# Kernel optimization log

Measured on AMD Instinct MI355X. Metric: run time of the kernel, lower is better.

## Reference

```python
import jax, jax.numpy as jnp
import numpy as np

N, E = 20000, 200000
HID, NH, L = 128, 8, 7
DH = HID // NH
SCALE = float(np.sqrt(DH))
NNUM = 5
MLP_IN = HID + HID + 8 + 8 + 8 + NNUM  # 285
EPS = 1e-5


def _ln(x, g, b):
    mu = jnp.mean(x, -1, keepdims=True)
    var = jnp.mean((x - mu) ** 2, -1, keepdims=True)
    return (x - mu) * jax.lax.rsqrt(var + EPS) * g + b


def setup_inputs() -> dict:
    key = jax.random.key(0)
    ks = jax.random.split(key, 24)
    f = lambda k, s: (0.05 * jax.random.normal(k, s)).astype(jnp.float32)
    z = lambda s: jnp.zeros(s, jnp.float32)
    o = lambda s: jnp.ones(s, jnp.float32)
    inp = {
        'node_feats': f(ks[0], (N, 2)),
        'numericals': f(ks[1], (E, NNUM)),
        'W_emb': f(ks[2], (2, HID)), 'b_emb': z((HID,)),
        'WQ': f(ks[3], (L, HID, HID)), 'bQ': z((L, HID)),
        'WK': f(ks[4], (L, HID, HID)), 'bK': z((L, HID)),
        'WV': f(ks[5], (L, HID, HID)), 'bV': z((L, HID)),
        'WO': f(ks[6], (L, HID, HID)), 'bO': z((L, HID)),
        'ln1_g': o((L, HID)), 'ln1_b': z((L, HID)),
        'ln2_g': o((L, HID)), 'ln2_b': z((L, HID)),
        'W1': f(ks[7], (L, HID, HID)), 'b1': z((L, HID)),
        'W2': f(ks[8], (L, HID, HID)), 'b2': z((L, HID)),
        'curr_emb': f(ks[9], (15, 8)), 'pay_emb': f(ks[10], (7, 8)),
        'mlp_Wh': f(ks[11], (3, MLP_IN, MLP_IN)), 'mlp_bh': z((3, MLP_IN)),
        'mlp_Wo': f(ks[12], (MLP_IN, 2)), 'mlp_bo': z((2,)),
        'src': jax.random.randint(ks[13], (E,), 0, N, dtype=jnp.int32),
        'dst': jax.random.randint(ks[14], (E,), 0, N, dtype=jnp.int32),
        'payment_currency': jax.random.randint(ks[15], (E,), 0, 15, dtype=jnp.int32),
        'receiving_currency': jax.random.randint(ks[16], (E,), 0, 15, dtype=jnp.int32),
        'payment_format': jax.random.randint(ks[17], (E,), 0, 7, dtype=jnp.int32),
    }
    return inp


def reference(node_feats, numericals, W_emb, b_emb, WQ, bQ, WK, bK, WV, bV, WO, bO,
              ln1_g, ln1_b, ln2_g, ln2_b, W1, b1, W2, b2, curr_emb, pay_emb,
              mlp_Wh, mlp_bh, mlp_Wo, mlp_bo, src, dst,
              payment_currency, receiving_currency, payment_format):
    h = node_feats @ W_emb + b_emb  # [N, HID]
    for l in range(L):
        # --- graph multi-head attention (segment softmax over in-edges of dst) ---
        x = _ln(h, ln1_g[l], ln1_b[l])
        Q = (x @ WQ[l] + bQ[l]).reshape(N, NH, DH)
        K = (x @ WK[l] + bK[l]).reshape(N, NH, DH)
        V = (x @ WV[l] + bV[l]).reshape(N, NH, DH)
        scores = jnp.einsum('ehd,ehd->eh', Q[dst], K[src]) / SCALE  # [E, NH]
        m = jax.ops.segment_max(scores, dst, num_segments=N)        # [N, NH]
        ex = jnp.exp(scores - m[dst])
        den = jax.ops.segment_sum(ex, dst, num_segments=N)
        w = ex / den[dst]                                           # attn weights per edge
        attn = jax.ops.segment_sum(w[:, :, None] * V[src], dst, num_segments=N)
        h = h + attn.reshape(N, HID) @ WO[l] + bO[l]
        # --- FFN ---
        x = _ln(h, ln2_g[l], ln2_b[l])
        h = h + jax.nn.relu(x @ W1[l] + b1[l]) @ W2[l] + b2[l]
    # --- edge classifier ---
    ef = jnp.concatenate([curr_emb[payment_currency], curr_emb[receiving_currency],
                          pay_emb[payment_format], numericals], axis=1)  # [E, 29]
    y = jnp.concatenate([h[src], h[dst], ef], axis=1)  # [E, 285]
    for i in range(3):
        y = jax.nn.relu(y @ mlp_Wh[i] + mlp_bh[i])
    return y @ mlp_Wo + mlp_bo  # [E, 2]
```

## Files before the change

kernel.cpp:

```cpp
#include <hip/hip_runtime.h>

#define HID 128
#define NH 8
#define DH 16
#define NLAYERS 7
#define MLP_IN 285
#define MP 288
#define LDW 296
#define XS 136

typedef short short8 __attribute__((ext_vector_type(8)));
typedef float f32x4 __attribute__((ext_vector_type(4)));
typedef float f32x16 __attribute__((ext_vector_type(16)));
typedef unsigned short ushort8 __attribute__((ext_vector_type(8)));

__device__ inline unsigned short f2bf(float f) {
    union { float f; unsigned int u; } v; v.f = f;
    unsigned int r = v.u + 0x7FFF + ((v.u >> 16) & 1);
    return (unsigned short)(r >> 16);
}
__device__ inline float bf2f(unsigned short u) {
    union { unsigned int u; float f; } v; v.u = ((unsigned int)u) << 16;
    return v.f;
}

__global__ __launch_bounds__(256) void embed_kernel(
    const float* __restrict__ nf, const float* __restrict__ We,
    const float* __restrict__ be, float* __restrict__ h, int N)
{
    int idx = blockIdx.x * 256 + threadIdx.x;
    if (idx >= N * HID) return;
    int n = idx >> 7, j = idx & 127;
    h[idx] = fmaf(nf[n * 2], We[j], fmaf(nf[n * 2 + 1], We[HID + j], be[j]));
}

__global__ __launch_bounds__(256) void prep_nodew_kernel(
    const float* __restrict__ WQ, const float* __restrict__ WK,
    const float* __restrict__ WV, const float* __restrict__ WO,
    const float* __restrict__ W1, const float* __restrict__ W2,
    unsigned short* __restrict__ wnh, unsigned short* __restrict__ wnl)
{
    int idx = blockIdx.x * 256 + threadIdx.x;
    if (idx >= 42 * 32 * 64) return;
    int lane = idx & 63;
    int r = idx >> 6;
    int kt = r & 7; r >>= 3;
    int ct = r & 3; r >>= 2;
    int m = r;
    int l = m / 6, wi = m - l * 6;
    const float* Wb;
    switch (wi) {
        case 0: Wb = WQ; break; case 1: Wb = WK; break; case 2: Wb = WV; break;
        case 3: Wb = WO; break; case 4: Wb = W1; break; default: Wb = W2; break;
    }
    Wb += (size_t)l * HID * HID;
    int n = ct * 32 + (lane & 31);
    int kb = kt * 16 + (lane >> 5) * 8;
    ushort8 vh, vl;
#pragma unroll
    for (int j = 0; j < 8; ++j) {
        float w = Wb[(size_t)(kb + j) * HID + n];
        unsigned short hi = f2bf(w);
        vh[j] = hi;
        vl[j] = f2bf(w - bf2f(hi));
    }
    *(ushort8*)&wnh[(size_t)idx * 8] = vh;
    *(ushort8*)&wnl[(size_t)idx * 8] = vl;
}

#define LOADB(m, BH, BL) do { \
    size_t fb_ = (((size_t)(matbase + (m)) * 32 + (size_t)wave * 8) * 64 + lane) * 8; \
    const unsigned short* Bh_ = wnh + fb_; \
    const unsigned short* Bl_ = wnl + fb_; \
    _Pragma("unroll") \
    for (int kt = 0; kt < 8; ++kt) { \
        BH[kt] = *(const short8*)&Bh_[kt * 512]; \
        BL[kt] = *(const short8*)&Bl_[kt * 512]; \
    } \
    __builtin_amdgcn_sched_barrier(0); \
} while (0)

#define COMPSTORE(BH, BL, BIAS, OUT, STRIDE, OFF) do { \
    f32x16 acc = {}; \
    _Pragma("unroll") \
    for (int kt = 0; kt < 8; ++kt) \
        acc = __builtin_amdgcn_mfma_f32_32x32x16_bf16(ah[kt], BH[kt], acc, 0, 0, 0); \
    _Pragma("unroll") \
    for (int kt = 0; kt < 8; ++kt) \
        acc = __builtin_amdgcn_mfma_f32_32x32x16_bf16(al[kt], BH[kt], acc, 0, 0, 0); \
    _Pragma("unroll") \
    for (int kt = 0; kt < 8; ++kt) \
        acc = __builtin_amdgcn_mfma_f32_32x32x16_bf16(ah[kt], BL[kt], acc, 0, 0, 0); \
    int col_ = wave * 32 + l31; \
    float bv_ = (BIAS)[col_]; \
    _Pragma("unroll") \
    for (int r = 0; r < 16; ++r) { \
        int rowm_ = (r & 3) + 8 * (r >> 2) + 4 * half; \
        int row_ = rowBase + rowm_; \
        if (row_ < M) (OUT)[(size_t)row_ * (STRIDE) + (OFF) + col_] = acc[r] + bv_; \
    } \
} while (0)

__global__ __launch_bounds__(256, 2) void ln_qkv_mfma(
    const float* __restrict__ h,
    const float* __restrict__ g, const float* __restrict__ bb,
    const unsigned short* __restrict__ wnh, const unsigned short* __restrict__ wnl,
    int matbase,
    const float* __restrict__ bQ, const float* __restrict__ bK, const float* __restrict__ bV,
    float* __restrict__ qo, float* __restrict__ kvo, int M)
{
    __shared__ unsigned short Xh[32][XS];
    __shared__ unsigned short Xl[32][XS];
    int tid = threadIdx.x;
    int lane = tid & 63, wave = tid >> 6;
    int rowBase = blockIdx.x * 32;

    for (int i = 0; i < 8; ++i) {
        int r = wave * 8 + i;
        int row = rowBase + r;
        float a0 = 0.f, a1 = 0.f;
        if (row < M) {
            a0 = h[(size_t)row * HID + lane];
            a1 = h[(size_t)row * HID + 64 + lane];
        }
        float s = a0 + a1;
#pragma unroll
        for (int off = 32; off > 0; off >>= 1) s += __shfl_down(s, off, 64);
        s = __shfl(s, 0, 64);
        float mu = s * (1.0f / 128.0f);
        float d0 = a0 - mu, d1 = a1 - mu;
        float v = d0 * d0 + d1 * d1;
#pragma unroll
        for (int off = 32; off > 0; off >>= 1) v += __shfl_down(v, off, 64);
        v = __shfl(v, 0, 64);
        float rr = rsqrtf(v * (1.0f / 128.0f) + 1e-5f);
        float x0 = d0 * rr * g[lane] + bb[lane];
        float x1 = d1 * rr * g[64 + lane] + bb[64 + lane];
        unsigned short h0 = f2bf(x0), h1 = f2bf(x1);
        Xh[r][lane] = h0;           Xh[r][64 + lane] = h1;
        Xl[r][lane] = f2bf(x0 - bf2f(h0));
        Xl[r][64 + lane] = f2bf(x1 - bf2f(h1));
    }
    __syncthreads();

    int l31 = lane & 31;
    int half = lane >> 5;

    short8 ah[8], al[8];
#pragma unroll
    for (int kt = 0; kt < 8; ++kt) {
        ah[kt] = *(const short8*)&Xh[l31][kt * 16 + half * 8];
        al[kt] = *(const short8*)&Xl[l31][kt * 16 + half * 8];
    }

    short8 bh0[8], bl0[8], bh1[8], bl1[8];
    LOADB(0, bh0, bl0);
    LOADB(1, bh1, bl1);
    COMPSTORE(bh0, bl0, bQ, qo, HID, 0);
    LOADB(2, bh0, bl0);
    COMPSTORE(bh1, bl1, bK, kvo, 256, 0);
    COMPSTORE(bh0, bl0, bV, kvo, 256, 128);
}

__global__ __launch_bounds__(256, 2) void post_qkv_mfma(
    const float* __restrict__ at, const float* __restrict__ hin,
    const unsigned short* __restrict__ wnh, const unsigned short* __restrict__ wnl,
    int matbase,
    const float* __restrict__ bO,
    const float* __restrict__ g2, const float* __restrict__ b2g,
    const float* __restrict__ b1, const float* __restrict__ b2,
    float* __restrict__ hout,
    int doQkv,
    const float* __restrict__ g1n, const float* __restrict__ b1n,
    const float* __restrict__ bQn, const float* __restrict__ bKn, const float* __restrict__ bVn,
    float* __restrict__ qout, float* __restrict__ kvout,
    unsigned short* __restrict__ hbout,
    int M)
{
    __shared__ unsigned short Ah[32][XS];
    __shared__ unsigned short Al[32][XS];
    __shared__ unsigned short Th[32][XS];
    __shared__ unsigned short Tl[32][XS];
    __shared__ float Hs[32][132];
    int tid = threadIdx.x;
    int lane = tid & 63, wave = tid >> 6;
    int rowBase = blockIdx.x * 32;
    int l31 = lane & 31;
    int half = lane >> 5;

    for (int i = tid; i < 32 * 32; i += 256) {
        int r = i >> 5, c4 = i & 31;
        int row = rowBase + r;
        float4 va = make_float4(0.f, 0.f, 0.f, 0.f), vh = va;
        if (row < M) {
            va = *(const float4*)&at[(size_t)row * HID + c4 * 4];
            vh = *(const float4*)&hin[(size_t)row * HID + c4 * 4];
        }
        const float* vp = (const float*)&va;
#pragma unroll
        for (int q = 0; q < 4; ++q) {
            unsigned short hi = f2bf(vp[q]);
            Ah[r][c4 * 4 + q] = hi;
            Al[r][c4 * 4 + q] = f2bf(vp[q] - bf2f(hi));
        }
        *(float4*)&Hs[r][c4 * 4] = vh;
    }
    __syncthreads();

    int colW = wave * 32 + l31;

    {
        short8 ah[8], al[8];
#pragma unroll
        for (int kt = 0; kt < 8; ++kt) {
            ah[kt] = *(const short8*)&Ah[l31][kt * 16 + half * 8];
            al[kt] = *(const short8*)&Al[l31][kt * 16 + half * 8];
        }
        short8 bh[8], bl[8];
        {
            size_t fb = (((size_t)(matbase + 3) * 32 + (size_t)wave * 8) * 64 + lane) * 8;
            const unsigned short* Bh = wnh + fb;
            const unsigned short* Bl = wnl + fb;
#pragma unroll
            for (int kt = 0; kt < 8; ++kt) {
                bh[kt] = *(const short8*)&Bh[kt * 512];
                bl[kt] = *(const short8*)&Bl[kt * 512];
            }
            __builtin_amdgcn_sched_barrier(0);
        }
        f32x16 acc = {};
#pragma unroll
        for (int kt = 0; kt < 8; ++kt)
            acc = __builtin_amdgcn_mfma_f32_32x32x16_bf16(ah[kt], bh[kt], acc, 0, 0, 0);
#pragma unroll
        for (int kt = 0; kt < 8; ++kt)
            acc = __builtin_amdgcn_mfma_f32_32x32x16_bf16(al[kt], bh[kt], acc, 0, 0, 0);
#pragma unroll
        for (int kt = 0; kt < 8; ++kt)
            acc = __builtin_amdgcn_mfma_f32_32x32x16_bf16(ah[kt], bl[kt], acc, 0, 0, 0);
        float bv = bO[colW];
#pragma unroll
        for (int r = 0; r < 16; ++r) {
            int rowm = (r & 3) + 8 * (r >> 2) + 4 * half;
            Hs[rowm][colW] += acc[r] + bv;
        }
    }
    __syncthreads();

    for (int i = 0; i < 8; ++i) {
        int r = wave * 8 + i;
        float a0 = Hs[r][lane];
        float a1 = Hs[r][64 + lane];
        float s = a0 + a1;
#pragma unroll
        for (int off = 32; off > 0; off >>= 1) s += __shfl_down(s, off, 64);
        s = __shfl(s, 0, 64);
        float mu = s * (1.0f / 128.0f);
        float d0 = a0 - mu, d1 = a1 - mu;
        float v = d0 * d0 + d1 * d1;
#pragma unroll
        for (int off = 32; off > 0; off >>= 1) v += __shfl_down(v, off, 64);
        v = __shfl(v, 0, 64);
        float rr = rsqrtf(v * (1.0f / 128.0f) + 1e-5f);
        float x0 = d0 * rr * g2[lane] + b2g[lane];
        float x1 = d1 * rr * g2[64 + lane] + b2g[64 + lane];
        unsigned short h0 = f2bf(x0), h1 = f2bf(x1);
        Ah[r][lane] = h0;           Ah[r][64 + lane] = h1;
        Al[r][lane] = f2bf(x0 - bf2f(h0));
        Al[r][64 + lane] = f2bf(x1 - bf2f(h1));
    }
    __syncthreads();

    {
        short8 ah[8], al[8];
#pragma unroll
        for (int kt = 0; kt < 8; ++kt) {
            ah[kt] = *(const short8*)&Ah[l31][kt * 16 + half * 8];
            al[kt] = *(const short8*)&Al[l31][kt * 16 + half * 8];
        }
        short8 bh[8], bl[8];
        {
            size_t fb = (((size_t)(matbase + 4) * 32 + (size_t)wave * 8) * 64 + lane) * 8;
            const unsigned short* Bh = wnh + fb;
            const unsigned short* Bl = wnl + fb;
#pragma unroll
            for (int kt = 0; kt < 8; ++kt) {
                bh[kt] = *(const short8*)&Bh[kt * 512];
                bl[kt] = *(const short8*)&Bl[kt * 512];
            }
            __builtin_amdgcn_sched_barrier(0);
        }
        f32x16 acc = {};
#pragma unroll
        for (int kt = 0; kt < 8; ++kt)
            acc = __builtin_amdgcn_mfma_f32_32x32x16_bf16(ah[kt], bh[kt], acc, 0, 0, 0);
#pragma unroll
        for (int kt = 0; kt < 8; ++kt)
            acc = __builtin_amdgcn_mfma_f32_32x32x16_bf16(al[kt], bh[kt], acc, 0, 0, 0);
#pragma unroll
        for (int kt = 0; kt < 8; ++kt)
            acc = __builtin_amdgcn_mfma_f32_32x32x16_bf16(ah[kt], bl[kt], acc, 0, 0, 0);
        float bv = b1[colW];
#pragma unroll
        for (int r = 0; r < 16; ++r) {
            int rowm = (r & 3) + 8 * (r >> 2) + 4 * half;
            float t = fmaxf(acc[r] + bv, 0.f);
            unsigned short hi = f2bf(t);
            Th[rowm][colW] = hi;
            Tl[rowm][colW] = f2bf(t - bf2f(hi));
        }
    }
    __syncthreads();

    {
        short8 ah[8], al[8];
#pragma unroll
        for (int kt = 0; kt < 8; ++kt) {
            ah[kt] = *(const short8*)&Th[l31][kt * 16 + half * 8];
            al[kt] = *(const short8*)&Tl[l31][kt * 16 + half * 8];
        }
        short8 bh[8], bl[8];
        {
            size_t fb = (((size_t)(matbase + 5) * 32 + (size_t)wave * 8) * 64 + lane) * 8;
            const unsigned short* Bh = wnh + fb;
            const unsigned short* Bl = wnl + fb;
#pragma unroll
            for (int kt = 0; kt < 8; ++kt) {
                bh[kt] = *(const short8*)&Bh[kt * 512];
                bl[kt] = *(const short8*)&Bl[kt * 512];
            }
            __builtin_amdgcn_sched_barrier(0);
        }
        f32x16 acc = {};
#pragma unroll
        for (int kt = 0; kt < 8; ++kt)
            acc = __builtin_amdgcn_mfma_f32_32x32x16_bf16(ah[kt], bh[kt], acc, 0, 0, 0);
#pragma unroll
        for (int kt = 0; kt < 8; ++kt)
            acc = __builtin_amdgcn_mfma_f32_32x32x16_bf16(al[kt], bh[kt], acc, 0, 0, 0);
#pragma unroll
        for (int kt = 0; kt < 8; ++kt)
            acc = __builtin_amdgcn_mfma_f32_32x32x16_bf16(ah[kt], bl[kt], acc, 0, 0, 0);
        float bv = b2[colW];
#pragma unroll
        for (int r = 0; r < 16; ++r) {
            int rowm = (r & 3) + 8 * (r >> 2) + 4 * half;
            int row = rowBase + rowm;
            float hn = Hs[rowm][colW] + acc[r] + bv;
            Hs[rowm][colW] = hn;
            if (row < M) {
                if (doQkv) hout[(size_t)row * HID + colW] = hn;
                else       hbout[(size_t)row * HID + colW] = f2bf(hn);
            }
        }
    }

    if (!doQkv) return;
    __syncthreads();

    for (int i = 0; i < 8; ++i) {
        int r = wave * 8 + i;
        float a0 = Hs[r][lane];
        float a1 = Hs[r][64 + lane];
        float s = a0 + a1;
#pragma unroll
        for (int off = 32; off > 0; off >>= 1) s += __shfl_down(s, off, 64);
        s = __shfl(s, 0, 64);
        float mu = s * (1.0f / 128.0f);
        float d0 = a0 - mu, d1 = a1 - mu;
        float v = d0 * d0 + d1 * d1;
#pragma unroll
        for (int off = 32; off > 0; off >>= 1) v += __shfl_down(v, off, 64);
        v = __shfl(v, 0, 64);
        float rr = rsqrtf(v * (1.0f / 128.0f) + 1e-5f);
        float x0 = d0 * rr * g1n[lane] + b1n[lane];
        float x1 = d1 * rr * g1n[64 + lane] + b1n[64 + lane];
        unsigned short h0 = f2bf(x0), h1 = f2bf(x1);
        Ah[r][lane] = h0;           Ah[r][64 + lane] = h1;
        Al[r][lane] = f2bf(x0 - bf2f(h0));
        Al[r][64 + lane] = f2bf(x1 - bf2f(h1));
    }
    __syncthreads();

    {
        short8 ah[8], al[8];
#pragma unroll
        for (int kt = 0; kt < 8; ++kt) {
            ah[kt] = *(const short8*)&Ah[l31][kt * 16 + half * 8];
            al[kt] = *(const short8*)&Al[l31][kt * 16 + half * 8];
        }
        short8 bh0[8], bl0[8], bh1[8], bl1[8];
        LOADB(6, bh0, bl0);
        LOADB(7, bh1, bl1);
        COMPSTORE(bh0, bl0, bQn, qout, HID, 0);
        LOADB(8, bh0, bl0);
        COMPSTORE(bh1, bl1, bKn, kvout, 256, 0);
        COMPSTORE(bh0, bl0, bVn, kvout, 256, 128);
    }
}

__global__ __launch_bounds__(256) void deg_kernel(
    const int* __restrict__ dst, int* __restrict__ deg, int E)
{
    int e = blockIdx.x * 256 + threadIdx.x;
    if (e < E) atomicAdd(&deg[dst[e]], 1);
}

__global__ __launch_bounds__(256) void scan_kernel(
    const int* __restrict__ deg, int* __restrict__ rowptr,
    int* __restrict__ cursor, int N)
{
    __shared__ int sums[256];
    int tid = threadIdx.x;
    int chunk = (N + 255) / 256;
    int lo = tid * chunk;
    int hi = lo + chunk; if (hi > N) hi = N;
    int s = 0;
    for (int i = lo; i < hi && i >= 0; ++i) s += deg[i];
    sums[tid] = s;
    __syncthreads();
    for (int off = 1; off < 256; off <<= 1) {
        int v = (tid >= off) ? sums[tid - off] : 0;
        __syncthreads();
        sums[tid] += v;
        __syncthreads();
    }
    int base = (tid == 0) ? 0 : sums[tid - 1];
    for (int i = lo; i < hi; ++i) {
        rowptr[i] = base; cursor[i] = base; base += deg[i];
    }
    if (tid == 255) rowptr[N] = sums[255];
}

__global__ __launch_bounds__(256) void scatter_kernel(
    const int* __restrict__ src, const int* __restrict__ dst,
    int* __restrict__ cursor, int* __restrict__ ssrc, int E)
{
    int e = blockIdx.x * 256 + threadIdx.x;
    if (e < E) {
        int p = atomicAdd(&cursor[dst[e]], 1);
        ssrc[p] = src[e];
    }
}

__global__ __launch_bounds__(256) void attn_fused_kernel(
    const float* __restrict__ q, const float* __restrict__ kv,
    const int* __restrict__ rowptr, const int* __restrict__ ssrc,
    float* __restrict__ at, int N)
{
    int node = blockIdx.x * 4 + (threadIdx.x >> 6);
    int lane = threadIdx.x & 63;
    if (node >= N) return;
    int beg = rowptr[node], end = rowptr[node + 1];
    float q0 = q[(size_t)node * HID + lane];
    float q1 = q[(size_t)node * HID + 64 + lane];
    float acc0 = 0.f, acc1 = 0.f, den0 = 0.f, den1 = 0.f;
    int i = beg;
    for (; i + 2 <= end; i += 2) {
        int s0 = ssrc[i], s1 = ssrc[i + 1];
        const float* kv0 = kv + (size_t)s0 * 256;
        const float* kv1 = kv + (size_t)s1 * 256;
        float k00 = kv0[lane],       k01 = kv0[64 + lane];
        float v00 = kv0[128 + lane], v01 = kv0[192 + lane];
        float k10 = kv1[lane],       k11 = kv1[64 + lane];
        float v10 = kv1[128 + lane], v11 = kv1[192 + lane];
        float p00 = q0 * k00, p01 = q1 * k01;
        float p10 = q0 * k10, p11 = q1 * k11;
#pragma unroll
        for (int off = 1; off < 16; off <<= 1) {
            p00 += __shfl_xor(p00, off, 64);
            p01 += __shfl_xor(p01, off, 64);
            p10 += __shfl_xor(p10, off, 64);
            p11 += __shfl_xor(p11, off, 64);
        }
        float w00 = __expf(p00 * 0.25f), w01 = __expf(p01 * 0.25f);
        float w10 = __expf(p10 * 0.25f), w11 = __expf(p11 * 0.25f);
        den0 += w00 + w10; den1 += w01 + w11;
        acc0 = fmaf(w10, v10, fmaf(w00, v00, acc0));
        acc1 = fmaf(w11, v11, fmaf(w01, v01, acc1));
    }
    if (i < end) {
        int s = ssrc[i];
        const float* kv0 = kv + (size_t)s * 256;
        float k0 = kv0[lane], k1 = kv0[64 + lane];
        float p0 = q0 * k0, p1 = q1 * k1;
#pragma unroll
        for (int off = 1; off < 16; off <<= 1) {
            p0 += __shfl_xor(p0, off, 64);
            p1 += __shfl_xor(p1, off, 64);
        }
        float w0 = __expf(p0 * 0.25f), w1 = __expf(p1 * 0.25f);
        den0 += w0; den1 += w1;
        acc0 = fmaf(w0, kv0[128 + lane], acc0);
        acc1 = fmaf(w1, kv0[192 + lane], acc1);
    }
    at[(size_t)node * HID + lane]      = (den0 > 0.f) ? acc0 / den0 : 0.f;
    at[(size_t)node * HID + 64 + lane] = (den1 > 0.f) ? acc1 / den1 : 0.f;
}

__global__ __launch_bounds__(256) void prep_wp_kernel(
    const float* __restrict__ Wh, unsigned short* __restrict__ wp)
{
    int idx = blockIdx.x * 256 + threadIdx.x;
    if (idx >= 3 * 9 * 18 * 64) return;
    int lane = idx & 63;
    int r = idx >> 6;
    int kt = r % 18; r /= 18;
    int ct = r % 9;
    int layer = r / 9;
    int n = ct * 32 + (lane & 31);
    int kbase = kt * 16 + (lane >> 5) * 8;
    ushort8 val;
#pragma unroll
    for (int j = 0; j < 8; ++j) {
        int k = kbase + j;
        float v = (n < MLP_IN && k < MLP_IN)
            ? Wh[(size_t)layer * MLP_IN * MLP_IN + (size_t)k * MLP_IN + n] : 0.f;
        val[j] = f2bf(v);
    }
    *(ushort8*)&wp[(size_t)idx * 8] = val;
}

__global__ __launch_bounds__(256, 2) void edge_mlp_mfma(
    const unsigned short* __restrict__ hb, const float* __restrict__ ce,
    const float* __restrict__ pe, const float* __restrict__ num,
    const int* __restrict__ src, const int* __restrict__ dst,
    const int* __restrict__ pc, const int* __restrict__ rc,
    const int* __restrict__ pf,
    const unsigned short* __restrict__ wp, const float* __restrict__ bh,
    const float* __restrict__ Wo, const float* __restrict__ bo,
    float* __restrict__ out, int E)
{
    __shared__ unsigned short y[64 * LDW];
    int tid = threadIdx.x;
    int e0 = blockIdx.x * 64;
    int wave = tid >> 6;
    int lane = tid & 63;
    int l31 = lane & 31;
    int half = lane >> 5;

    for (int i = tid; i < 64 * 36; i += 256) {
        int t = i / 36;
        int c = i - t * 36;
        int e = e0 + t;
        if (e >= E) e = E - 1;
        ushort8 val;
        if (c < 16) {
            val = *(const ushort8*)&hb[(size_t)src[e] * HID + c * 8];
        } else if (c < 32) {
            val = *(const ushort8*)&hb[(size_t)dst[e] * HID + (c - 16) * 8];
        } else if (c == 32) {
            const float* p = &ce[pc[e] * 8];
#pragma unroll
            for (int j = 0; j < 8; ++j) val[j] = f2bf(p[j]);
        } else if (c == 33) {
            const float* p = &ce[rc[e] * 8];
#pragma unroll
            for (int j = 0; j < 8; ++j) val[j] = f2bf(p[j]);
        } else if (c == 34) {
            const float* p = &pe[pf[e] * 8];
#pragma unroll
            for (int j = 0; j < 8; ++j) val[j] = f2bf(p[j]);
        } else {
            const float* p = &num[(size_t)e * 5];
#pragma unroll
            for (int j = 0; j < 5; ++j) val[j] = f2bf(p[j]);
            val[5] = 0; val[6] = 0; val[7] = 0;
        }
        *(ushort8*)&y[t * LDW + c * 8] = val;
    }
    __syncthreads();

    int slab = wave >> 1;
    int rowA = slab * 32 + l31;
    int ctlo = (wave & 1) ? 5 : 0;
    int cthi = (wave & 1) ? 9 : 5;

    for (int layer = 0; layer < 3; ++layer) {
        const float* __restrict__ bias = bh + layer * MLP_IN;

        short8 afr[18];
#pragma unroll
        for (int kt = 0; kt < 18; ++kt)
            afr[kt] = *(const short8*)&y[rowA * LDW + kt * 16 + half * 8];
        __syncthreads();

        for (int ct = ctlo; ct < cthi; ++ct) {
            const unsigned short* __restrict__ Bp =
                wp + (size_t)layer * 82944 + (size_t)ct * 9216 + (size_t)lane * 8;
            short8 bfr[18];
#pragma unroll
            for (int kt = 0; kt < 18; ++kt)
                bfr[kt] = *(const short8*)&Bp[kt * 512];
            __builtin_amdgcn_sched_barrier(0);
            f32x16 acc = {};
#pragma unroll
            for (int kt = 0; kt < 18; ++kt)
                acc = __builtin_amdgcn_mfma_f32_32x32x16_bf16(afr[kt], bfr[kt], acc, 0, 0, 0);
            int col = ct * 32 + l31;
            if (col < MLP_IN) {
                float bv = bias[col];
#pragma unroll
                for (int r = 0; r < 16; ++r) {
                    int rowm = (r & 3) + 8 * (r >> 2) + 4 * half;
                    float t = fmaxf(acc[r] + bv, 0.f);
                    y[(slab * 32 + rowm) * LDW + col] = f2bf(t);
                }
            }
        }
        __syncthreads();
    }

    {
        int t = tid >> 2;
        int oc = tid & 1;
        int kk = (tid >> 1) & 1;
        int e = e0 + t;
        const unsigned short* yr = &y[t * LDW];
        float p0 = 0.f, p1 = 0.f, p2 = 0.f, p3 = 0.f;
        int kc_lo = kk ? 18 : 0;
        int kc_hi = kk ? 35 : 18;
        for (int kc = kc_lo; kc < kc_hi; ++kc) {
            ushort8 yv = *(const ushort8*)&yr[kc * 8];
            int kb = kc * 8;
            p0 = fmaf(bf2f(yv[0]), Wo[(kb + 0) * 2 + oc], p0);
            p1 = fmaf(bf2f(yv[1]), Wo[(kb + 1) * 2 + oc], p1);
            p2 = fmaf(bf2f(yv[2]), Wo[(kb + 2) * 2 + oc], p2);
            p3 = fmaf(bf2f(yv[3]), Wo[(kb + 3) * 2 + oc], p3);
            p0 = fmaf(bf2f(yv[4]), Wo[(kb + 4) * 2 + oc], p0);
            p1 = fmaf(bf2f(yv[5]), Wo[(kb + 5) * 2 + oc], p1);
            p2 = fmaf(bf2f(yv[6]), Wo[(kb + 6) * 2 + oc], p2);
            p3 = fmaf(bf2f(yv[7]), Wo[(kb + 7) * 2 + oc], p3);
        }
        float acc = (p0 + p1) + (p2 + p3);
        if (kk) {
            for (int k = 280; k < MLP_IN; ++k)
                acc = fmaf(bf2f(yr[k]), Wo[k * 2 + oc], acc);
        }
        acc += __shfl_xor(acc, 2, 64);
        if (kk == 0 && e < E)
            out[(size_t)e * 2 + oc] = acc + bo[oc];
    }
}

extern "C" void kernel_launch(void* const* d_in, const int* in_sizes, int n_in,
                              void* d_out, int out_size, void* d_ws, size_t ws_size,
                              hipStream_t stream)
{
    const float* node_feats = (const float*)d_in[0];
    const float* numericals = (const float*)d_in[1];
    const float* W_emb = (const float*)d_in[2];
    const float* b_emb = (const float*)d_in[3];
    const float* WQ = (const float*)d_in[4];
    const float* bQ = (const float*)d_in[5];
    const float* WK = (const float*)d_in[6];
    const float* bK = (const float*)d_in[7];
    const float* WV = (const float*)d_in[8];
    const float* bV = (const float*)d_in[9];
    const float* WO = (const float*)d_in[10];
    const float* bO = (const float*)d_in[11];
    const float* ln1_g = (const float*)d_in[12];
    const float* ln1_b = (const float*)d_in[13];
    const float* ln2_g = (const float*)d_in[14];
    const float* ln2_b = (const float*)d_in[15];
    const float* W1 = (const float*)d_in[16];
    const float* b1 = (const float*)d_in[17];
    const float* W2 = (const float*)d_in[18];
    const float* b2 = (const float*)d_in[19];
    const float* curr_emb = (const float*)d_in[20];
    const float* pay_emb = (const float*)d_in[21];
    const float* mlp_Wh = (const float*)d_in[22];
    const float* mlp_bh = (const float*)d_in[23];
    const float* mlp_Wo = (const float*)d_in[24];
    const float* mlp_bo = (const float*)d_in[25];
    const int* src = (const int*)d_in[26];
    const int* dst = (const int*)d_in[27];
    const int* pc = (const int*)d_in[28];
    const int* rc = (const int*)d_in[29];
    const int* pf = (const int*)d_in[30];

    const int N = in_sizes[0] / 2;
    const int E = in_sizes[26];

    float* ws = (float*)d_ws;
    float* h    = ws;
    float* qb0  = h    + (size_t)N * HID;
    float* kvb0 = qb0  + (size_t)N * HID;
    float* qb1  = kvb0 + (size_t)N * HID * 2;
    float* kvb1 = qb1  + (size_t)N * HID;
    float* at   = kvb1 + (size_t)N * HID * 2;
    unsigned short* hb = (unsigned short*)(at + (size_t)N * HID);
    unsigned short* wpk = hb + (size_t)N * HID;
    unsigned short* wnh = wpk + (size_t)3 * 9 * 18 * 64 * 8;
    unsigned short* wnl = wnh + (size_t)42 * 32 * 64 * 8;
    int* rowptr = (int*)(wnl + (size_t)42 * 32 * 64 * 8);
    int* deg    = rowptr + (N + 1);
    int* cursor = deg + N;
    int* ssrc   = cursor + N;

    prep_wp_kernel<<<(3 * 9 * 18 * 64 + 255) / 256, 256, 0, stream>>>(mlp_Wh, wpk);
    prep_nodew_kernel<<<(42 * 32 * 64 + 255) / 256, 256, 0, stream>>>(
        WQ, WK, WV, WO, W1, W2, wnh, wnl);

    embed_kernel<<<(N * HID + 255) / 256, 256, 0, stream>>>(node_feats, W_emb, b_emb, h, N);

    hipMemsetAsync(deg, 0, (size_t)N * sizeof(int), stream);
    deg_kernel<<<(E + 255) / 256, 256, 0, stream>>>(dst, deg, E);
    scan_kernel<<<1, 256, 0, stream>>>(deg, rowptr, cursor, N);
    scatter_kernel<<<(E + 255) / 256, 256, 0, stream>>>(src, dst, cursor, ssrc, E);

    int nodeBlocks = (N + 31) / 32;

    ln_qkv_mfma<<<nodeBlocks, 256, 0, stream>>>(
        h, ln1_g, ln1_b, wnh, wnl, 0,
        bQ, bK, bV, qb0, kvb0, N);

    float* qbuf[2]  = { qb0, qb1 };
    float* kvbuf[2] = { kvb0, kvb1 };

    for (int l = 0; l < NLAYERS; ++l) {
        int cur = l & 1, nxt = cur ^ 1;
        int doQkv = (l < NLAYERS - 1) ? 1 : 0;
        int ln = (l + 1 < NLAYERS) ? (l + 1) : 0;

        attn_fused_kernel<<<(N + 3) / 4, 256, 0, stream>>>(
            qbuf[cur], kvbuf[cur], rowptr, ssrc, at, N);

        post_qkv_mfma<<<nodeBlocks, 256, 0, stream>>>(
            at, h, wnh, wnl, l * 6,
            bO + l * HID,
            ln2_g + l * HID, ln2_b + l * HID,
            b1 + l * HID, b2 + l * HID,
            h, doQkv,
            ln1_g + ln * HID, ln1_b + ln * HID,
            bQ + ln * HID, bK + ln * HID, bV + ln * HID,
            qbuf[nxt], kvbuf[nxt],
            hb, N);
    }

    edge_mlp_mfma<<<(E + 63) / 64, 256, 0, stream>>>(
        hb, curr_emb, pay_emb, numericals, src, dst, pc, rc, pf,
        wpk, mlp_bh, mlp_Wo, mlp_bo, (float*)d_out, E);
}
```

Measured before the change: 1.077 ms.

## Double-buffer MLP weight tiles in LDS via async global-to-LDS loads, 128 edges per block

The edge MLP kernel now handles 128 edges per block, with each wave owning a 32-row slab and computing all 9 column tiles. It used to handle 64 edges, with waves splitting the column tiles. Weight column tiles are prefetched into a double-buffered LDS area with global_load_lds while the current tile is being multiplied, so all waves share one weight fetch. The aim is to cut redundant per-wave global weight reads and hide their latency. In exchange, LDS use grows to about 110 KB, which may reduce occupancy, and there is now a block barrier after every column tile.

```diff
diff --git a/kernel.cpp b/kernel.cpp
--- a/kernel.cpp
+++ b/kernel.cpp
@@ -22,6 +22,13 @@
 __device__ inline float bf2f(unsigned short u) {
     union { unsigned int u; float f; } v; v.u = ((unsigned int)u) << 16;
     return v.f;
+}
+
+__device__ inline void gload_lds16(const void* gptr, void* lptr) {
+    __builtin_amdgcn_global_load_lds(
+        (const __attribute__((address_space(1))) unsigned int*)gptr,
+        (__attribute__((address_space(3))) unsigned int*)lptr,
+        16, 0, 0);
 }
 
 __global__ __launch_bounds__(256) void embed_kernel(
@@ -531,15 +538,23 @@
     const float* __restrict__ Wo, const float* __restrict__ bo,
     float* __restrict__ out, int E)
 {
-    __shared__ unsigned short y[64 * LDW];
+    __shared__ unsigned short y[128 * LDW];
+    __shared__ unsigned short Bs[2][9216];
     int tid = threadIdx.x;
-    int e0 = blockIdx.x * 64;
+    int e0 = blockIdx.x * 128;
     int wave = tid >> 6;
     int lane = tid & 63;
     int l31 = lane & 31;
     int half = lane >> 5;
 
-    for (int i = tid; i < 64 * 36; i += 256) {
+    {
+        const char* gsrc = (const char*)wp;
+        char* ldst = (char*)&Bs[0][0];
+        for (int c = wave; c < 18; c += 4)
+            gload_lds16(gsrc + c * 1024 + lane * 16, ldst + c * 1024);
+    }
+
+    for (int i = tid; i < 128 * 36; i += 256) {
         int t = i / 36;
         int c = i - t * 36;
         int e = e0 + t;
@@ -569,12 +584,11 @@
         }
         *(ushort8*)&y[t * LDW + c * 8] = val;
     }
-    __syncthreads();
-
-    int slab = wave >> 1;
-    int rowA = slab * 32 + l31;
-    int ctlo = (wave & 1) ? 5 : 0;
-    int cthi = (wave & 1) ? 9 : 5;
+    asm volatile("s_waitcnt vmcnt(0)" ::: "memory");
+    __syncthreads();
+
+    int rowA = wave * 32 + l31;
+    int buf = 0;
 
     for (int layer = 0; layer < 3; ++layer) {
         const float* __restrict__ bias = bh + layer * MLP_IN;
@@ -583,20 +597,24 @@
 #pragma unroll
         for (int kt = 0; kt < 18; ++kt)
             afr[kt] = *(const short8*)&y[rowA * LDW + kt * 16 + half * 8];
-        __syncthreads();
-
-        for (int ct = ctlo; ct < cthi; ++ct) {
-            const unsigned short* __restrict__ Bp =
-                wp + (size_t)layer * 82944 + (size_t)ct * 9216 + (size_t)lane * 8;
-            short8 bfr[18];
-#pragma unroll
-            for (int kt = 0; kt < 18; ++kt)
-                bfr[kt] = *(const short8*)&Bp[kt * 512];
-            __builtin_amdgcn_sched_barrier(0);
+
+        for (int ct = 0; ct < 9; ++ct) {
+            int nl = layer, nct = ct + 1;
+            if (nct == 9) { nl = layer + 1; nct = 0; }
+            if (nl < 3) {
+                const char* gsrc = (const char*)wp
+                    + ((size_t)nl * 82944 + (size_t)nct * 9216) * 2;
+                char* ldst = (char*)&Bs[buf ^ 1][0];
+                for (int c = wave; c < 18; c += 4)
+                    gload_lds16(gsrc + c * 1024 + lane * 16, ldst + c * 1024);
+            }
+
             f32x16 acc = {};
 #pragma unroll
-            for (int kt = 0; kt < 18; ++kt)
-                acc = __builtin_amdgcn_mfma_f32_32x32x16_bf16(afr[kt], bfr[kt], acc, 0, 0, 0);
+            for (int kt = 0; kt < 18; ++kt) {
+                short8 bfr = *(const short8*)&Bs[buf][kt * 512 + lane * 8];
+                acc = __builtin_amdgcn_mfma_f32_32x32x16_bf16(afr[kt], bfr, acc, 0, 0, 0);
+            }
             int col = ct * 32 + l31;
             if (col < MLP_IN) {
                 float bv = bias[col];
@@ -604,42 +622,39 @@
                 for (int r = 0; r < 16; ++r) {
                     int rowm = (r & 3) + 8 * (r >> 2) + 4 * half;
                     float t = fmaxf(acc[r] + bv, 0.f);
-                    y[(slab * 32 + rowm) * LDW + col] = f2bf(t);
+                    y[(wave * 32 + rowm) * LDW + col] = f2bf(t);
                 }
             }
-        }
-        __syncthreads();
+
+            asm volatile("s_waitcnt vmcnt(0)" ::: "memory");
+            __syncthreads();
+            buf ^= 1;
+        }
     }
 
     {
-        int t = tid >> 2;
-        int oc = tid & 1;
-        int kk = (tid >> 1) & 1;
+        int t = tid >> 1, oc = tid & 1;
         int e = e0 + t;
-        const unsigned short* yr = &y[t * LDW];
-        float p0 = 0.f, p1 = 0.f, p2 = 0.f, p3 = 0.f;
-        int kc_lo = kk ? 18 : 0;
-        int kc_hi = kk ? 35 : 18;
-        for (int kc = kc_lo; kc < kc_hi; ++kc) {
-            ushort8 yv = *(const ushort8*)&yr[kc * 8];
-            int kb = kc * 8;
-            p0 = fmaf(bf2f(yv[0]), Wo[(kb + 0) * 2 + oc], p0);
-            p1 = fmaf(bf2f(yv[1]), Wo[(kb + 1) * 2 + oc], p1);
-            p2 = fmaf(bf2f(yv[2]), Wo[(kb + 2) * 2 + oc], p2);
-            p3 = fmaf(bf2f(yv[3]), Wo[(kb + 3) * 2 + oc], p3);
-            p0 = fmaf(bf2f(yv[4]), Wo[(kb + 4) * 2 + oc], p0);
-            p1 = fmaf(bf2f(yv[5]), Wo[(kb + 5) * 2 + oc], p1);
-            p2 = fmaf(bf2f(yv[6]), Wo[(kb + 6) * 2 + oc], p2);
-            p3 = fmaf(bf2f(yv[7]), Wo[(kb + 7) * 2 + oc], p3);
-        }
-        float acc = (p0 + p1) + (p2 + p3);
-        if (kk) {
+        if (e < E) {
+            const unsigned short* yr = &y[t * LDW];
+            float p0 = 0.f, p1 = 0.f, p2 = 0.f, p3 = 0.f;
+            for (int kc = 0; kc < 35; ++kc) {
+                ushort8 yv = *(const ushort8*)&yr[kc * 8];
+                int kb = kc * 8;
+                p0 = fmaf(bf2f(yv[0]), Wo[(kb + 0) * 2 + oc], p0);
+                p1 = fmaf(bf2f(yv[1]), Wo[(kb + 1) * 2 + oc], p1);
+                p2 = fmaf(bf2f(yv[2]), Wo[(kb + 2) * 2 + oc], p2);
+                p3 = fmaf(bf2f(yv[3]), Wo[(kb + 3) * 2 + oc], p3);
+                p0 = fmaf(bf2f(yv[4]), Wo[(kb + 4) * 2 + oc], p0);
+                p1 = fmaf(bf2f(yv[5]), Wo[(kb + 5) * 2 + oc], p1);
+                p2 = fmaf(bf2f(yv[6]), Wo[(kb + 6) * 2 + oc], p2);
+                p3 = fmaf(bf2f(yv[7]), Wo[(kb + 7) * 2 + oc], p3);
+            }
+            float acc = bo[oc] + (p0 + p1) + (p2 + p3);
             for (int k = 280; k < MLP_IN; ++k)
                 acc = fmaf(bf2f(yr[k]), Wo[k * 2 + oc], acc);
-        }
-        acc += __shfl_xor(acc, 2, 64);
-        if (kk == 0 && e < E)
-            out[(size_t)e * 2 + oc] = acc + bo[oc];
+            out[(size_t)e * 2 + oc] = acc;
+        }
     }
 }
 
@@ -738,7 +753,7 @@
             hb, N);
     }
 
-    edge_mlp_mfma<<<(E + 63) / 64, 256, 0, stream>>>(
+    edge_mlp_mfma<<<(E + 127) / 128, 256, 0, stream>>>(
         hb, curr_emb, pay_emb, numericals, src, dst, pc, rc, pf,
         wpk, mlp_bh, mlp_Wo, mlp_bo, (float*)d_out, E);
 }
```

After: 1.201 ms. 1.11x slower.

## Split each node's in-edges across two waves and raise edge MLP occupancy

Applied to the files above, without the earlier changes.

The attention kernel now gives each destination node two wavefronts, each handling half of its in-edge list, and combines the partial accumulators and denominators through shared memory before normalising. This doubles the parallelism and memory-level concurrency for the irregular gather, at the cost of a block barrier and a shared-memory reduction. The edge MLP kernel's launch bounds are raised from 2 to 4 blocks per SM, and a scheduling barrier between its B-fragment loads and the MFMA chain is removed. Together these aim for more occupancy and overlap, but the tighter register budget may cause spills given the 18-entry fragment arrays.

```diff
diff --git a/kernel.cpp b/kernel.cpp
--- a/kernel.cpp
+++ b/kernel.cpp
@@ -448,54 +448,76 @@
     const int* __restrict__ rowptr, const int* __restrict__ ssrc,
     float* __restrict__ at, int N)
 {
-    int node = blockIdx.x * 4 + (threadIdx.x >> 6);
-    int lane = threadIdx.x & 63;
-    if (node >= N) return;
-    int beg = rowptr[node], end = rowptr[node + 1];
-    float q0 = q[(size_t)node * HID + lane];
-    float q1 = q[(size_t)node * HID + 64 + lane];
+    __shared__ float red[2][2][4][64];
+    int tid = threadIdx.x;
+    int wv = tid >> 6;
+    int lane = tid & 63;
+    int slot = wv >> 1;
+    int hf = wv & 1;
+    int node = blockIdx.x * 2 + slot;
+
     float acc0 = 0.f, acc1 = 0.f, den0 = 0.f, den1 = 0.f;
-    int i = beg;
-    for (; i + 2 <= end; i += 2) {
-        int s0 = ssrc[i], s1 = ssrc[i + 1];
-        const float* kv0 = kv + (size_t)s0 * 256;
-        const float* kv1 = kv + (size_t)s1 * 256;
-        float k00 = kv0[lane],       k01 = kv0[64 + lane];
-        float v00 = kv0[128 + lane], v01 = kv0[192 + lane];
-        float k10 = kv1[lane],       k11 = kv1[64 + lane];
-        float v10 = kv1[128 + lane], v11 = kv1[192 + lane];
-        float p00 = q0 * k00, p01 = q1 * k01;
-        float p10 = q0 * k10, p11 = q1 * k11;
-#pragma unroll
-        for (int off = 1; off < 16; off <<= 1) {
-            p00 += __shfl_xor(p00, off, 64);
-            p01 += __shfl_xor(p01, off, 64);
-            p10 += __shfl_xor(p10, off, 64);
-            p11 += __shfl_xor(p11, off, 64);
-        }
-        float w00 = __expf(p00 * 0.25f), w01 = __expf(p01 * 0.25f);
-        float w10 = __expf(p10 * 0.25f), w11 = __expf(p11 * 0.25f);
-        den0 += w00 + w10; den1 += w01 + w11;
-        acc0 = fmaf(w10, v10, fmaf(w00, v00, acc0));
-        acc1 = fmaf(w11, v11, fmaf(w01, v01, acc1));
-    }
-    if (i < end) {
-        int s = ssrc[i];
-        const float* kv0 = kv + (size_t)s * 256;
-        float k0 = kv0[lane], k1 = kv0[64 + lane];
-        float p0 = q0 * k0, p1 = q1 * k1;
-#pragma unroll
-        for (int off = 1; off < 16; off <<= 1) {
-            p0 += __shfl_xor(p0, off, 64);
-            p1 += __shfl_xor(p1, off, 64);
-        }
-        float w0 = __expf(p0 * 0.25f), w1 = __expf(p1 * 0.25f);
-        den0 += w0; den1 += w1;
-        acc0 = fmaf(w0, kv0[128 + lane], acc0);
-        acc1 = fmaf(w1, kv0[192 + lane], acc1);
-    }
-    at[(size_t)node * HID + lane]      = (den0 > 0.f) ? acc0 / den0 : 0.f;
-    at[(size_t)node * HID + 64 + lane] = (den1 > 0.f) ? acc1 / den1 : 0.f;
+    if (node < N) {
+        int beg = rowptr[node], end = rowptr[node + 1];
+        int lenA = (end - beg + 1) >> 1;
+        int b = hf ? (beg + lenA) : beg;
+        int e = hf ? end : (beg + lenA);
+        float q0 = q[(size_t)node * HID + lane];
+        float q1 = q[(size_t)node * HID + 64 + lane];
+        int i = b;
+        for (; i + 2 <= e; i += 2) {
+            int s0 = ssrc[i], s1 = ssrc[i + 1];
+            const float* kv0 = kv + (size_t)s0 * 256;
+            const float* kv1 = kv + (size_t)s1 * 256;
+            float k00 = kv0[lane],       k01 = kv0[64 + lane];
+            float v00 = kv0[128 + lane], v01 = kv0[192 + lane];
+            float k10 = kv1[lane],       k11 = kv1[64 + lane];
+            float v10 = kv1[128 + lane], v11 = kv1[192 + lane];
+            float p00 = q0 * k00, p01 = q1 * k01;
+            float p10 = q0 * k10, p11 = q1 * k11;
+#pragma unroll
+            for (int off = 1; off < 16; off <<= 1) {
+                p00 += __shfl_xor(p00, off, 64);
+                p01 += __shfl_xor(p01, off, 64);
+                p10 += __shfl_xor(p10, off, 64);
+                p11 += __shfl_xor(p11, off, 64);
+            }
+            float w00 = __expf(p00 * 0.25f), w01 = __expf(p01 * 0.25f);
+            float w10 = __expf(p10 * 0.25f), w11 = __expf(p11 * 0.25f);
+            den0 += w00 + w10; den1 += w01 + w11;
+            acc0 = fmaf(w10, v10, fmaf(w00, v00, acc0));
+            acc1 = fmaf(w11, v11, fmaf(w01, v01, acc1));
+        }
+        if (i < e) {
+            int s = ssrc[i];
+            const float* kv0 = kv + (size_t)s * 256;
+            float k0 = kv0[lane], k1 = kv0[64 + lane];
+            float p0 = q0 * k0, p1 = q1 * k1;
+#pragma unroll
+            for (int off = 1; off < 16; off <<= 1) {
+                p0 += __shfl_xor(p0, off, 64);
+                p1 += __shfl_xor(p1, off, 64);
+            }
+            float w0 = __expf(p0 * 0.25f), w1 = __expf(p1 * 0.25f);
+            den0 += w0; den1 += w1;
+            acc0 = fmaf(w0, kv0[128 + lane], acc0);
+            acc1 = fmaf(w1, kv0[192 + lane], acc1);
+        }
+    }
+    red[slot][hf][0][lane] = acc0;
+    red[slot][hf][1][lane] = acc1;
+    red[slot][hf][2][lane] = den0;
+    red[slot][hf][3][lane] = den1;
+    __syncthreads();
+
+    if (hf == 0 && node < N) {
+        float a0 = red[slot][0][0][lane] + red[slot][1][0][lane];
+        float a1 = red[slot][0][1][lane] + red[slot][1][1][lane];
+        float d0 = red[slot][0][2][lane] + red[slot][1][2][lane];
+        float d1 = red[slot][0][3][lane] + red[slot][1][3][lane];
+        at[(size_t)node * HID + lane]      = (d0 > 0.f) ? a0 / d0 : 0.f;
+        at[(size_t)node * HID + 64 + lane] = (d1 > 0.f) ? a1 / d1 : 0.f;
+    }
 }
 
 __global__ __launch_bounds__(256) void prep_wp_kernel(
@@ -521,7 +543,7 @@
     *(ushort8*)&wp[(size_t)idx * 8] = val;
 }
 
-__global__ __launch_bounds__(256, 2) void edge_mlp_mfma(
+__global__ __launch_bounds__(256, 4) void edge_mlp_mfma(
     const unsigned short* __restrict__ hb, const float* __restrict__ ce,
     const float* __restrict__ pe, const float* __restrict__ num,
     const int* __restrict__ src, const int* __restrict__ dst,
@@ -592,7 +614,6 @@
 #pragma unroll
             for (int kt = 0; kt < 18; ++kt)
                 bfr[kt] = *(const short8*)&Bp[kt * 512];
-            __builtin_amdgcn_sched_barrier(0);
             f32x16 acc = {};
 #pragma unroll
             for (int kt = 0; kt < 18; ++kt)
@@ -723,7 +744,7 @@
         int doQkv = (l < NLAYERS - 1) ? 1 : 0;
         int ln = (l + 1 < NLAYERS) ? (l + 1) : 0;
 
-        attn_fused_kernel<<<(N + 3) / 4, 256, 0, stream>>>(
+        attn_fused_kernel<<<(N + 1) / 2, 256, 0, stream>>>(
             qbuf[cur], kvbuf[cur], rowptr, ssrc, at, N);
 
         post_qkv_mfma<<<nodeBlocks, 256, 0, stream>>>(
```

Result: faster. 1.010 ms (-6.2%).
